# Kernel optimization log

Hardware: AMD Instinct MI355X
Metric: run time of the kernel (lower is better)

The kernel has to match this reference:

```python
import jax, jax.numpy as jnp
import numpy as np

N, DIN, DOUT, E, K = 65536, 256, 256, 8, 2

def setup_inputs() -> dict:
    key = jax.random.key(0)
    k1, k2, k3, k4 = jax.random.split(key, 4)
    x = jax.random.normal(k1, (N, DIN), dtype=jnp.float32)
    Wr = jax.random.normal(k2, (DIN, E), dtype=jnp.float32) * (DIN ** -0.5)   # router Linear (no bias)
    We = jax.random.normal(k3, (E, DIN, DOUT), dtype=jnp.float32) * (DIN ** -0.5)  # expert Linear weights
    be = jax.random.normal(k4, (E, DOUT), dtype=jnp.float32) * 0.01               # expert Linear biases
    return {"x": x, "Wr": Wr, "We": We, "be": be}

def reference(x, Wr, We, be):
    # router: softmax over experts (eval mode -> no noise)
    probs = jax.nn.softmax(x @ Wr, axis=1)                    # [N, E]
    w, sel = jax.lax.top_k(probs, K)                          # [N, K]
    w = w / jnp.sum(w, axis=1, keepdims=True)                 # renormalize top-k weights
    # dense combine weights: scatter top-k weights back to [N, E]
    combine = jnp.zeros_like(probs).at[jnp.arange(x.shape[0])[:, None], sel].add(w)
    # all-expert outputs, then weighted combine (same math as gather/matmul/index_add loop)
    y_all = jnp.einsum('ni,eio->neo', x, We) + be[None, :, :]  # [N, E, DOUT]
    out = jnp.einsum('neo,ne->no', y_all, combine)             # [N, DOUT]
    return out
```

## Files before the change

### kernel.cpp

```cpp
#include <hip/hip_runtime.h>

#define N_TOK 65536
#define DIN   256
#define DOUT  256
#define NEXP  8
#define NPAIR 28

typedef __bf16 bf16x8 __attribute__((ext_vector_type(8)));
typedef float  f32x4  __attribute__((ext_vector_type(4)));

__global__ __launch_bounds__(256) void prep_kernel(const float* __restrict__ We,
                                                   __bf16* __restrict__ Wt,
                                                   int* __restrict__ cnt) {
  int idx = blockIdx.x * 256 + threadIdx.x;
  if (blockIdx.x == 0 && threadIdx.x < NPAIR) cnt[threadIdx.x] = 0;
  int e = idx >> 16;
  int r = idx & 0xFFFF;
  int n = r >> 8;
  int k = r & 0xFF;
  Wt[idx] = (__bf16)We[(e << 16) + (k << 8) + n];
}

__global__ __launch_bounds__(64) void router_kernel(const float* __restrict__ x,
                                                    const float* __restrict__ Wr,
                                                    int* __restrict__ cnt,
                                                    unsigned short* __restrict__ pidx,
                                                    float* __restrict__ pw) {
  __shared__ float WrL[DIN * NEXP];
  __shared__ int lcnt[NPAIR];
  __shared__ int gbase[NPAIR];
  int tid = threadIdx.x;
  for (int j = tid; j < DIN * NEXP / 4; j += 64)
    *(float4*)&WrL[j * 4] = *(const float4*)&Wr[j * 4];
  if (tid < NPAIR) lcnt[tid] = 0;
  __syncthreads();

  int token = blockIdx.x * 64 + tid;
  const float4* xr = (const float4*)(x + (size_t)token * DIN);
  double acc[NEXP];
#pragma unroll
  for (int e = 0; e < NEXP; e++) acc[e] = 0.0;

#pragma unroll 2
  for (int i4 = 0; i4 < DIN / 4; i4++) {
    float4 xv = xr[i4];
#pragma unroll
    for (int u = 0; u < 4; u++) {
      float xf = (u == 0) ? xv.x : (u == 1) ? xv.y : (u == 2) ? xv.z : xv.w;
      double xd = (double)xf;
      const float* wrow = &WrL[(i4 * 4 + u) * NEXP];
#pragma unroll
      for (int e = 0; e < NEXP; e++) acc[e] = fma(xd, (double)wrow[e], acc[e]);
    }
  }

  int best = 0;
#pragma unroll
  for (int e = 1; e < NEXP; e++) if (acc[e] > acc[best]) best = e;
  int sec = (best == 0) ? 1 : 0;
#pragma unroll
  for (int e = 0; e < NEXP; e++)
    if (e != best && e != sec && acc[e] > acc[sec]) sec = e;

  float wb = 1.f / (1.f + expf((float)(acc[sec] - acc[best])));
  int a, b; float wa;
  if (best < sec) { a = best; b = sec; wa = wb; }
  else           { a = sec;  b = best; wa = 1.f - wb; }
  int p = a * (15 - a) / 2 + (b - a - 1);

  int lpos = atomicAdd(&lcnt[p], 1);
  __syncthreads();
  if (tid < NPAIR) gbase[tid] = atomicAdd(&cnt[tid], lcnt[tid]);
  __syncthreads();
  int pos = gbase[p] + lpos;
  pidx[p * N_TOK + pos] = (unsigned short)token;
  pw[p * N_TOK + pos] = wa;
}

__device__ inline bf16x8 cvt8(float4 a, float4 b, float s) {
  bf16x8 v;
  v[0] = (__bf16)(a.x * s); v[1] = (__bf16)(a.y * s);
  v[2] = (__bf16)(a.z * s); v[3] = (__bf16)(a.w * s);
  v[4] = (__bf16)(b.x * s); v[5] = (__bf16)(b.y * s);
  v[6] = (__bf16)(b.z * s); v[7] = (__bf16)(b.w * s);
  return v;
}

__global__ __launch_bounds__(256) void moe_gemm_kernel(const float* __restrict__ x,
                                                       const __bf16* __restrict__ Wt,
                                                       const float* __restrict__ be,
                                                       const int* __restrict__ cnt,
                                                       const unsigned short* __restrict__ pidx,
                                                       const float* __restrict__ pw,
                                                       float* __restrict__ out) {
  __shared__ __bf16 As[128 * 72];
  __shared__ __bf16 Bs[128 * 72];
  __shared__ unsigned short tokL[128];
  __shared__ float wL[128];
  __shared__ int meta[4];

  int tid = threadIdx.x;
  int tile = blockIdx.x >> 1;
  int nh = blockIdx.x & 1;

  if (tid == 0) {
    int s = 0, p = -1, lt = 0, c = 0;
    for (int q = 0; q < NPAIR; q++) {
      int cq = cnt[q];
      int tq = (cq + 127) >> 7;
      if (tile < s + tq) { p = q; lt = tile - s; c = cq; break; }
      s += tq;
    }
    meta[0] = p; meta[1] = lt; meta[2] = c;
  }
  __syncthreads();
  int p = meta[0];
  if (p < 0) return;
  int lt = meta[1], cnt_p = meta[2];

  int a = 0, rem = p;
  while (rem >= 7 - a) { rem -= 7 - a; a++; }
  int b = a + 1 + rem;
  int r0 = lt * 128;

  if (tid < 128) {
    int gr = r0 + tid;
    unsigned short t = 0; float wv = 0.f;
    if (gr < cnt_p) { t = pidx[p * N_TOK + gr]; wv = pw[p * N_TOK + gr]; }
    tokL[tid] = t; wL[tid] = wv;
  }
  __syncthreads();

  const int lane = tid & 63, wid = tid >> 6;
  const int wm = wid & 1, wn = wid >> 1;
  const int c16 = lane & 15, quad = lane >> 4;

  f32x4 acc[4][4];
#pragma unroll
  for (int mi = 0; mi < 4; mi++)
#pragma unroll
    for (int ni = 0; ni < 4; ni++)
#pragma unroll
      for (int r = 0; r < 4; r++) acc[mi][ni][r] = 0.f;

  const int rowA = tid >> 1, segA = tid & 1;

  for (int kc = 0; kc < 8; kc++) {
    int kx = (kc & 3) * 64;
    int eSel = (kc < 4) ? a : b;
    {
      float wrow = wL[rowA];
      if (kc >= 4) wrow = 1.f - wrow;
      const float4* src = (const float4*)(x + (size_t)tokL[rowA] * DIN + kx + segA * 32);
      float4 f0 = src[0], f1 = src[1], f2 = src[2], f3 = src[3];
      float4 f4 = src[4], f5 = src[5], f6 = src[6], f7 = src[7];
      __bf16* dst = &As[rowA * 72 + segA * 32];
      *(bf16x8*)(dst + 0)  = cvt8(f0, f1, wrow);
      *(bf16x8*)(dst + 8)  = cvt8(f2, f3, wrow);
      *(bf16x8*)(dst + 16) = cvt8(f4, f5, wrow);
      *(bf16x8*)(dst + 24) = cvt8(f6, f7, wrow);
    }
    {
      const int4* bsrc = (const int4*)(Wt + (size_t)((eSel * 256 + nh * 128 + rowA) * 256) + kx + segA * 32);
      int4* dstb = (int4*)&Bs[rowA * 72 + segA * 32];
      dstb[0] = bsrc[0]; dstb[1] = bsrc[1]; dstb[2] = bsrc[2]; dstb[3] = bsrc[3];
    }
    __syncthreads();
#pragma unroll
    for (int ks = 0; ks < 2; ks++) {
      bf16x8 af[4], bfv[4];
#pragma unroll
      for (int mi = 0; mi < 4; mi++)
        af[mi] = *(const bf16x8*)&As[(wm * 64 + mi * 16 + c16) * 72 + ks * 32 + quad * 8];
#pragma unroll
      for (int ni = 0; ni < 4; ni++)
        bfv[ni] = *(const bf16x8*)&Bs[(wn * 64 + ni * 16 + c16) * 72 + ks * 32 + quad * 8];
#pragma unroll
      for (int mi = 0; mi < 4; mi++)
#pragma unroll
        for (int ni = 0; ni < 4; ni++)
          acc[mi][ni] = __builtin_amdgcn_mfma_f32_16x16x32_bf16(af[mi], bfv[ni], acc[mi][ni], 0, 0, 0);
    }
    __syncthreads();
  }

#pragma unroll
  for (int ni = 0; ni < 4; ni++) {
    int gcol = nh * 128 + wn * 64 + ni * 16 + c16;
    float bea = be[a * DOUT + gcol];
    float beb = be[b * DOUT + gcol];
#pragma unroll
    for (int mi = 0; mi < 4; mi++) {
#pragma unroll
      for (int r = 0; r < 4; r++) {
        int row = wm * 64 + mi * 16 + quad * 4 + r;
        if (r0 + row < cnt_p) {
          float wa = wL[row];
          float v = acc[mi][ni][r] + wa * bea + (1.f - wa) * beb;
          out[(size_t)tokL[row] * DOUT + gcol] = v;
        }
      }
    }
  }
}

extern "C" void kernel_launch(void* const* d_in, const int* in_sizes, int n_in,
                              void* d_out, int out_size, void* d_ws, size_t ws_size,
                              hipStream_t stream) {
  const float* x  = (const float*)d_in[0];
  const float* Wr = (const float*)d_in[1];
  const float* We = (const float*)d_in[2];
  const float* be = (const float*)d_in[3];
  float* out = (float*)d_out;

  char* w = (char*)d_ws;
  __bf16* Wt = (__bf16*)w;
  int* cnt = (int*)(w + (1 << 20));
  unsigned short* pidx = (unsigned short*)(w + (1 << 20) + 512);
  float* pw = (float*)(w + (1 << 20) + 512 + (size_t)NPAIR * N_TOK * 2);

  prep_kernel<<<2048, 256, 0, stream>>>(We, Wt, cnt);
  router_kernel<<<N_TOK / 64, 64, 0, stream>>>(x, Wr, cnt, pidx, pw);
  moe_gemm_kernel<<<540 * 2, 256, 0, stream>>>(x, Wt, be, cnt, pidx, pw, out);
}
```

Measured before the change: 229.2 us.

## Rework router, prep transpose, and MoE GEMM with bf16 x copy and async LDS loads

The prep kernel now transposes the expert weights through a shared-memory tile so reads and writes are coalesced. The router runs in fp32 instead of fp64, with an fp64 recompute only when the second and third expert logits are close. It also writes a bf16 copy of x. The GEMM loads that bf16 x with global_load_lds into an XOR-swizzled LDS tile and reads B fragments straight from global memory. It computes both experts separately with unscaled x and combines them in the epilogue, with N split into four 64-column tiles. This cuts the fp64 router cost and the fp32 gather/convert in the GEMM, at the price of an extra 32 MB bf16 write and read and uncached B-operand global loads.

```diff
diff --git a/kernel.cpp b/kernel.cpp
--- a/kernel.cpp
+++ b/kernel.cpp
@@ -7,51 +7,73 @@
 #define NPAIR 28
 
 typedef __bf16 bf16x8 __attribute__((ext_vector_type(8)));
+typedef __bf16 bf16x4 __attribute__((ext_vector_type(4)));
 typedef float  f32x4  __attribute__((ext_vector_type(4)));
+
+__device__ __forceinline__ void cp16_g2l(const void* g, void* l) {
+  auto gp = (const __attribute__((address_space(1))) unsigned int*)(unsigned long long)g;
+  auto lp = (__attribute__((address_space(3))) unsigned int*)(unsigned long long)l;
+  __builtin_amdgcn_global_load_lds(gp, lp, 16, 0, 0);
+}
 
 __global__ __launch_bounds__(256) void prep_kernel(const float* __restrict__ We,
                                                    __bf16* __restrict__ Wt,
                                                    int* __restrict__ cnt) {
-  int idx = blockIdx.x * 256 + threadIdx.x;
-  if (blockIdx.x == 0 && threadIdx.x < NPAIR) cnt[threadIdx.x] = 0;
-  int e = idx >> 16;
-  int r = idx & 0xFFFF;
-  int n = r >> 8;
-  int k = r & 0xFF;
-  Wt[idx] = (__bf16)We[(e << 16) + (k << 8) + n];
-}
-
-__global__ __launch_bounds__(64) void router_kernel(const float* __restrict__ x,
-                                                    const float* __restrict__ Wr,
-                                                    int* __restrict__ cnt,
-                                                    unsigned short* __restrict__ pidx,
-                                                    float* __restrict__ pw) {
+  __shared__ float T[64 * 65];
+  int bid = blockIdx.x;
+  if (bid == 0 && threadIdx.x < NPAIR) cnt[threadIdx.x] = 0;
+  int e = bid >> 4;
+  int tk = (bid >> 2) & 3, tn = bid & 3;
+  int k0 = tk * 64, n0 = tn * 64;
+  int tid = threadIdx.x;
+  int cr = tid >> 6;
+  int cc = tid & 63;
+#pragma unroll
+  for (int i = 0; i < 16; i++) {
+    int k = i * 4 + cr;
+    T[cc * 65 + k] = We[(size_t)(e * 256 + k0 + k) * 256 + n0 + cc];
+  }
+  __syncthreads();
+#pragma unroll
+  for (int i = 0; i < 16; i++) {
+    int n = i * 4 + cr;
+    Wt[(size_t)(e * 256 + n0 + n) * 256 + k0 + cc] = (__bf16)T[n * 65 + cc];
+  }
+}
+
+__global__ __launch_bounds__(256) void router_kernel(const float* __restrict__ x,
+                                                     const float* __restrict__ Wr,
+                                                     __bf16* __restrict__ xb,
+                                                     int* __restrict__ cnt,
+                                                     unsigned short* __restrict__ pidx,
+                                                     float* __restrict__ pw) {
   __shared__ float WrL[DIN * NEXP];
   __shared__ int lcnt[NPAIR];
   __shared__ int gbase[NPAIR];
   int tid = threadIdx.x;
-  for (int j = tid; j < DIN * NEXP / 4; j += 64)
+  for (int j = tid; j < DIN * NEXP / 4; j += 256)
     *(float4*)&WrL[j * 4] = *(const float4*)&Wr[j * 4];
   if (tid < NPAIR) lcnt[tid] = 0;
   __syncthreads();
 
-  int token = blockIdx.x * 64 + tid;
+  int token = blockIdx.x * 256 + tid;
   const float4* xr = (const float4*)(x + (size_t)token * DIN);
-  double acc[NEXP];
-#pragma unroll
-  for (int e = 0; e < NEXP; e++) acc[e] = 0.0;
-
-#pragma unroll 2
+  __bf16* xbr = xb + (size_t)token * DIN;
+
+  float acc[NEXP];
+#pragma unroll
+  for (int e = 0; e < NEXP; e++) acc[e] = 0.f;
+
+#pragma unroll 8
   for (int i4 = 0; i4 < DIN / 4; i4++) {
-    float4 xv = xr[i4];
-#pragma unroll
-    for (int u = 0; u < 4; u++) {
-      float xf = (u == 0) ? xv.x : (u == 1) ? xv.y : (u == 2) ? xv.z : xv.w;
-      double xd = (double)xf;
-      const float* wrow = &WrL[(i4 * 4 + u) * NEXP];
-#pragma unroll
-      for (int e = 0; e < NEXP; e++) acc[e] = fma(xd, (double)wrow[e], acc[e]);
-    }
+    float4 v = xr[i4];
+    bf16x4 bv;
+    bv[0] = (__bf16)v.x; bv[1] = (__bf16)v.y; bv[2] = (__bf16)v.z; bv[3] = (__bf16)v.w;
+    *(bf16x4*)(xbr + i4 * 4) = bv;
+    const float* w0 = &WrL[(i4 * 4) * NEXP];
+#pragma unroll
+    for (int e = 0; e < NEXP; e++)
+      acc[e] += v.x * w0[e] + v.y * w0[NEXP + e] + v.z * w0[2 * NEXP + e] + v.w * w0[3 * NEXP + e];
   }
 
   int best = 0;
@@ -61,12 +83,42 @@
 #pragma unroll
   for (int e = 0; e < NEXP; e++)
     if (e != best && e != sec && acc[e] > acc[sec]) sec = e;
-
-  float wb = 1.f / (1.f + expf((float)(acc[sec] - acc[best])));
-  int a, b; float wa;
-  if (best < sec) { a = best; b = sec; wa = wb; }
-  else           { a = sec;  b = best; wa = 1.f - wb; }
-  int p = a * (15 - a) / 2 + (b - a - 1);
+  float l3 = -1e30f;
+#pragma unroll
+  for (int e = 0; e < NEXP; e++)
+    if (e != best && e != sec) l3 = fmaxf(l3, acc[e]);
+
+  float diff = acc[sec] - acc[best];
+  bool need = (acc[sec] - l3) < 5e-3f;
+  if (__any(need)) {
+    if (need) {
+      double d[NEXP];
+#pragma unroll
+      for (int e = 0; e < NEXP; e++) d[e] = 0.0;
+      for (int i4 = 0; i4 < DIN / 4; i4++) {
+        float4 v = xr[i4];
+        const float* w0 = &WrL[(i4 * 4) * NEXP];
+#pragma unroll
+        for (int e = 0; e < NEXP; e++)
+          d[e] += (double)v.x * w0[e] + (double)v.y * w0[NEXP + e] +
+                  (double)v.z * w0[2 * NEXP + e] + (double)v.w * w0[3 * NEXP + e];
+      }
+      best = 0;
+#pragma unroll
+      for (int e = 1; e < NEXP; e++) if (d[e] > d[best]) best = e;
+      sec = (best == 0) ? 1 : 0;
+#pragma unroll
+      for (int e = 0; e < NEXP; e++)
+        if (e != best && e != sec && d[e] > d[sec]) sec = e;
+      diff = (float)(d[sec] - d[best]);
+    }
+  }
+
+  float wb = 1.f / (1.f + expf(diff));
+  int a, b2; float wa;
+  if (best < sec) { a = best; b2 = sec; wa = wb; }
+  else            { a = sec;  b2 = best; wa = 1.f - wb; }
+  int p = a * (15 - a) / 2 + (b2 - a - 1);
 
   int lpos = atomicAdd(&lcnt[p], 1);
   __syncthreads();
@@ -77,41 +129,31 @@
   pw[p * N_TOK + pos] = wa;
 }
 
-__device__ inline bf16x8 cvt8(float4 a, float4 b, float s) {
-  bf16x8 v;
-  v[0] = (__bf16)(a.x * s); v[1] = (__bf16)(a.y * s);
-  v[2] = (__bf16)(a.z * s); v[3] = (__bf16)(a.w * s);
-  v[4] = (__bf16)(b.x * s); v[5] = (__bf16)(b.y * s);
-  v[6] = (__bf16)(b.z * s); v[7] = (__bf16)(b.w * s);
-  return v;
-}
-
-__global__ __launch_bounds__(256) void moe_gemm_kernel(const float* __restrict__ x,
+__global__ __launch_bounds__(256) void moe_gemm_kernel(const __bf16* __restrict__ xb,
                                                        const __bf16* __restrict__ Wt,
                                                        const float* __restrict__ be,
                                                        const int* __restrict__ cnt,
                                                        const unsigned short* __restrict__ pidx,
                                                        const float* __restrict__ pw,
                                                        float* __restrict__ out) {
-  __shared__ __bf16 As[128 * 72];
-  __shared__ __bf16 Bs[128 * 72];
+  __shared__ __bf16 As[128 * 64];
   __shared__ unsigned short tokL[128];
   __shared__ float wL[128];
   __shared__ int meta[4];
 
   int tid = threadIdx.x;
-  int tile = blockIdx.x >> 1;
-  int nh = blockIdx.x & 1;
+  int tile = blockIdx.x >> 2;
+  int nh = blockIdx.x & 3;
 
   if (tid == 0) {
-    int s = 0, p = -1, lt = 0, c = 0;
+    int s = 0, pp = -1, lt = 0, c = 0;
     for (int q = 0; q < NPAIR; q++) {
       int cq = cnt[q];
       int tq = (cq + 127) >> 7;
-      if (tile < s + tq) { p = q; lt = tile - s; c = cq; break; }
+      if (tile < s + tq) { pp = q; lt = tile - s; c = cq; break; }
       s += tq;
     }
-    meta[0] = p; meta[1] = lt; meta[2] = c;
+    meta[0] = pp; meta[1] = lt; meta[2] = c;
   }
   __syncthreads();
   int p = meta[0];
@@ -120,14 +162,13 @@
 
   int a = 0, rem = p;
   while (rem >= 7 - a) { rem -= 7 - a; a++; }
-  int b = a + 1 + rem;
+  int b2 = a + 1 + rem;
   int r0 = lt * 128;
 
   if (tid < 128) {
     int gr = r0 + tid;
-    unsigned short t = 0; float wv = 0.f;
-    if (gr < cnt_p) { t = pidx[p * N_TOK + gr]; wv = pw[p * N_TOK + gr]; }
-    tokL[tid] = t; wL[tid] = wv;
+    tokL[tid] = (gr < cnt_p) ? pidx[p * N_TOK + gr] : (unsigned short)0;
+    wL[tid]   = (gr < cnt_p) ? pw[p * N_TOK + gr] : 0.f;
   }
   __syncthreads();
 
@@ -135,69 +176,73 @@
   const int wm = wid & 1, wn = wid >> 1;
   const int c16 = lane & 15, quad = lane >> 4;
 
-  f32x4 acc[4][4];
+  const int r_base = tid >> 3;
+  const int s8 = (tid & 7) ^ (r_base & 7);
+  size_t grow[4];
+#pragma unroll
+  for (int i = 0; i < 4; i++)
+    grow[i] = (size_t)tokL[r_base + 32 * i] * DIN + s8 * 8;
+
+  const __bf16* WtA = Wt + ((size_t)a * DOUT + nh * 64) * DIN;
+  const __bf16* WtB = Wt + ((size_t)b2 * DOUT + nh * 64) * DIN;
+
+  f32x4 accA[4][2], accB[4][2];
 #pragma unroll
   for (int mi = 0; mi < 4; mi++)
 #pragma unroll
-    for (int ni = 0; ni < 4; ni++)
-#pragma unroll
-      for (int r = 0; r < 4; r++) acc[mi][ni][r] = 0.f;
-
-  const int rowA = tid >> 1, segA = tid & 1;
-
-  for (int kc = 0; kc < 8; kc++) {
-    int kx = (kc & 3) * 64;
-    int eSel = (kc < 4) ? a : b;
-    {
-      float wrow = wL[rowA];
-      if (kc >= 4) wrow = 1.f - wrow;
-      const float4* src = (const float4*)(x + (size_t)tokL[rowA] * DIN + kx + segA * 32);
-      float4 f0 = src[0], f1 = src[1], f2 = src[2], f3 = src[3];
-      float4 f4 = src[4], f5 = src[5], f6 = src[6], f7 = src[7];
-      __bf16* dst = &As[rowA * 72 + segA * 32];
-      *(bf16x8*)(dst + 0)  = cvt8(f0, f1, wrow);
-      *(bf16x8*)(dst + 8)  = cvt8(f2, f3, wrow);
-      *(bf16x8*)(dst + 16) = cvt8(f4, f5, wrow);
-      *(bf16x8*)(dst + 24) = cvt8(f6, f7, wrow);
-    }
-    {
-      const int4* bsrc = (const int4*)(Wt + (size_t)((eSel * 256 + nh * 128 + rowA) * 256) + kx + segA * 32);
-      int4* dstb = (int4*)&Bs[rowA * 72 + segA * 32];
-      dstb[0] = bsrc[0]; dstb[1] = bsrc[1]; dstb[2] = bsrc[2]; dstb[3] = bsrc[3];
-    }
+    for (int ni = 0; ni < 2; ni++)
+#pragma unroll
+      for (int r = 0; r < 4; r++) { accA[mi][ni][r] = 0.f; accB[mi][ni][r] = 0.f; }
+
+  for (int kc = 0; kc < 4; kc++) {
+#pragma unroll
+    for (int i = 0; i < 4; i++) {
+      int slot = tid + 256 * i;
+      cp16_g2l(xb + grow[i] + kc * 64, &As[slot * 8]);
+    }
+    __builtin_amdgcn_s_waitcnt(0x0F70);
     __syncthreads();
 #pragma unroll
     for (int ks = 0; ks < 2; ks++) {
-      bf16x8 af[4], bfv[4];
+      bf16x8 af[4], ba[2], bb[2];
+#pragma unroll
+      for (int mi = 0; mi < 4; mi++) {
+        int row = wm * 64 + mi * 16 + c16;
+        int oct = ks * 4 + quad;
+        af[mi] = *(const bf16x8*)&As[(row * 8 + (oct ^ (row & 7))) * 8];
+      }
+#pragma unroll
+      for (int ni = 0; ni < 2; ni++) {
+        int col = wn * 32 + ni * 16 + c16;
+        int koff = kc * 64 + ks * 32 + quad * 8;
+        ba[ni] = *(const bf16x8*)&WtA[(size_t)col * DIN + koff];
+        bb[ni] = *(const bf16x8*)&WtB[(size_t)col * DIN + koff];
+      }
 #pragma unroll
       for (int mi = 0; mi < 4; mi++)
-        af[mi] = *(const bf16x8*)&As[(wm * 64 + mi * 16 + c16) * 72 + ks * 32 + quad * 8];
-#pragma unroll
-      for (int ni = 0; ni < 4; ni++)
-        bfv[ni] = *(const bf16x8*)&Bs[(wn * 64 + ni * 16 + c16) * 72 + ks * 32 + quad * 8];
-#pragma unroll
-      for (int mi = 0; mi < 4; mi++)
-#pragma unroll
-        for (int ni = 0; ni < 4; ni++)
-          acc[mi][ni] = __builtin_amdgcn_mfma_f32_16x16x32_bf16(af[mi], bfv[ni], acc[mi][ni], 0, 0, 0);
+#pragma unroll
+        for (int ni = 0; ni < 2; ni++) {
+          accA[mi][ni] = __builtin_amdgcn_mfma_f32_16x16x32_bf16(af[mi], ba[ni], accA[mi][ni], 0, 0, 0);
+          accB[mi][ni] = __builtin_amdgcn_mfma_f32_16x16x32_bf16(af[mi], bb[ni], accB[mi][ni], 0, 0, 0);
+        }
     }
     __syncthreads();
   }
 
 #pragma unroll
-  for (int ni = 0; ni < 4; ni++) {
-    int gcol = nh * 128 + wn * 64 + ni * 16 + c16;
+  for (int ni = 0; ni < 2; ni++) {
+    int gcol = nh * 64 + wn * 32 + ni * 16 + c16;
     float bea = be[a * DOUT + gcol];
-    float beb = be[b * DOUT + gcol];
+    float beb = be[b2 * DOUT + gcol];
 #pragma unroll
     for (int mi = 0; mi < 4; mi++) {
 #pragma unroll
       for (int r = 0; r < 4; r++) {
         int row = wm * 64 + mi * 16 + quad * 4 + r;
         if (r0 + row < cnt_p) {
-          float wa = wL[row];
-          float v = acc[mi][ni][r] + wa * bea + (1.f - wa) * beb;
-          out[(size_t)tokL[row] * DOUT + gcol] = v;
+          float w = wL[row];
+          out[(size_t)tokL[row] * DOUT + gcol] =
+              w * (accA[mi][ni][r] + bea) + (1.f - w) * (accB[mi][ni][r] + beb);
         }
       }
     }
@@ -215,11 +260,12 @@
 
   char* w = (char*)d_ws;
   __bf16* Wt = (__bf16*)w;
-  int* cnt = (int*)(w + (1 << 20));
-  unsigned short* pidx = (unsigned short*)(w + (1 << 20) + 512);
-  float* pw = (float*)(w + (1 << 20) + 512 + (size_t)NPAIR * N_TOK * 2);
-
-  prep_kernel<<<2048, 256, 0, stream>>>(We, Wt, cnt);
-  router_kernel<<<N_TOK / 64, 64, 0, stream>>>(x, Wr, cnt, pidx, pw);
-  moe_gemm_kernel<<<540 * 2, 256, 0, stream>>>(x, Wt, be, cnt, pidx, pw, out);
-}
+  __bf16* xb = (__bf16*)(w + (1u << 20));
+  int* cnt = (int*)(w + (33u << 20));
+  unsigned short* pidx = (unsigned short*)(w + (33u << 20) + 512);
+  float* pw = (float*)(w + (33u << 20) + 512 + (size_t)NPAIR * N_TOK * 2);
+
+  prep_kernel<<<128, 256, 0, stream>>>(We, Wt, cnt);
+  router_kernel<<<N_TOK / 256, 256, 0, stream>>>(x, Wr, xb, cnt, pidx, pw);
+  moe_gemm_kernel<<<540 * 4, 256, 0, stream>>>(xb, Wt, be, cnt, pidx, pw, out);
+}
```

New measurement: 224.1 us. 2.2% less time.
